# Optimization experiments

Hardware: AMD Instinct MI355X
Metric: run time of the kernel (lower is better)

## Reference

```python
import jax, jax.numpy as jnp
import numpy as np

N, F, D, E, L, T = 20000, 512, 256, 200000, 3, 2  # nodes, raw feat, hidden, edges/etype, layers, etypes


def _layernorm(x, g, b, eps=1e-5):
    mu = jnp.mean(x, axis=-1, keepdims=True)
    var = jnp.mean(jnp.square(x - mu), axis=-1, keepdims=True)
    return (x - mu) * jax.lax.rsqrt(var + eps) * g + b


def setup_inputs() -> dict:
    key = jax.random.key(0)
    ks = jax.random.split(key, 12)
    s = 0.02
    return {
        "x": jax.random.normal(ks[0], (N, F), dtype=jnp.float32),
        "src": jax.random.randint(ks[1], (T, E), 0, N, dtype=jnp.int32),
        "dst": jax.random.randint(ks[2], (T, E), 0, N, dtype=jnp.int32),
        # HeteroLinear (single ntype)
        "Wlin": jax.random.normal(ks[3], (D, F), dtype=jnp.float32) * s,
        "blin": jnp.zeros((D,), dtype=jnp.float32),
        # stacked per-layer, per-etype SAGEConv('pool') params
        "Wpool": jax.random.normal(ks[4], (L, T, D, D), dtype=jnp.float32) * s,
        "bpool": jnp.zeros((L, T, D), dtype=jnp.float32),
        "Wself": jax.random.normal(ks[5], (L, T, D, D), dtype=jnp.float32) * s,
        "Wneigh": jax.random.normal(ks[6], (L, T, D, D), dtype=jnp.float32) * s,
        "bconv": jnp.zeros((L, T, D), dtype=jnp.float32),
        "gamma": jnp.ones((L, T, D), dtype=jnp.float32),
        "beta": jnp.zeros((L, T, D), dtype=jnp.float32),
    }


def reference(x, src, dst, Wlin, blin, Wpool, bpool, Wself, Wneigh, bconv, gamma, beta):
    n = x.shape[0]
    # HeteroLinear: raw features -> embed
    h = x @ Wlin.T + blin
    for l in range(L):
        out = None
        for t in range(T):  # per edge-type SAGEConv, aggregator='pool'
            hp = jax.nn.relu(h @ Wpool[l, t].T + bpool[l, t])        # fc_pool + relu on src nodes
            m = hp[src[t]]                                            # gather [E, D]
            neigh = jax.ops.segment_max(m, dst[t], num_segments=n)    # max-pool reduce
            neigh = jnp.where(jnp.isneginf(neigh), 0.0, neigh)        # zero-in-degree -> 0 (DGL)
            rst = h @ Wself[l, t].T + neigh @ Wneigh[l, t].T + bconv[l, t]
            if l < L - 1:
                rst = jax.nn.relu(rst)                                # activation before norm
            rst = _layernorm(rst, gamma[l, t], beta[l, t])
            out = rst if out is None else out + rst                   # HeteroGraphConv 'sum'
        h = out
    return h
```

## Files before the change

kernel.cpp:

```cpp
#include <hip/hip_runtime.h>

#define N_NODES 20000
#define F_IN    512
#define D_H     256
#define E_EDGES 200000
#define L_LAYERS 3
#define T_ETYPES 2
#define NBANDS  157
#define M_PAD   (NBANDS * 128)

typedef __attribute__((ext_vector_type(8))) short bf16x8;
typedef __attribute__((ext_vector_type(4))) float f32x4;

__device__ __forceinline__ unsigned short f2b(float f) {
    unsigned int u = __float_as_uint(f);
    u = (u + 0x7FFFu + ((u >> 16) & 1u)) >> 16;
    return (unsigned short)u;
}
__device__ __forceinline__ unsigned int pack2(float a, float b) {
    return (unsigned int)f2b(a) | ((unsigned int)f2b(b) << 16);
}

__device__ __forceinline__ void gload16(const unsigned short* g, unsigned short* l)
{
    __builtin_amdgcn_global_load_lds(
        (const __attribute__((address_space(1))) void*)g,
        (__attribute__((address_space(3))) void*)l, 16, 0, 0);
}

__device__ __forceinline__ size_t slab_addr(int row, int col, int kslabs)
{
    return ((size_t)(row >> 7) * kslabs + (col >> 5)) * 4096
         + (((row >> 4) & 7) << 9) + (((col >> 3) & 3) << 7)
         + ((row & 15) << 3) + (col & 7);
}

__device__ __forceinline__ void shufg8(const float* __restrict__ s,
                                       unsigned short* __restrict__ d,
                                       int NO, int Mreal, int K, int o8)
{
    const int matsz8 = (NO * K) >> 3;
    const int mat = o8 / matsz8;
    const int rem = o8 - mat * matsz8;
    const int dst = rem << 3;
    const int slab = dst >> 12;
    const int w = dst & 4095;
    const int spr = K >> 5;
    const int slab_n = slab / spr, slab_k = slab - slab_n * spr;
    int row = slab_n * 128 + (((w >> 9) & 7) << 4) + ((w >> 3) & 15);
    if (row >= Mreal) row = Mreal - 1;
    const int kk = ((w >> 7) & 3) << 3;
    const size_t soff = (size_t)mat * Mreal * K + (size_t)row * K + slab_k * 32 + kk;
    const float4 a = *(const float4*)(s + soff);
    const float4 b = *(const float4*)(s + soff + 4);
    uint4 u;
    u.x = pack2(a.x, a.y); u.y = pack2(a.z, a.w);
    u.z = pack2(b.x, b.y); u.w = pack2(b.z, b.w);
    *(uint4*)(d + (size_t)mat * NO * K + dst) = u;
}

__global__ __launch_bounds__(256) void prep_kernel(
    const float* __restrict__ x,  unsigned short* __restrict__ xb, int nx8,
    const float* __restrict__ s0, unsigned short* __restrict__ d0, int NO0, int K0, int n08,
    const float* __restrict__ s1, unsigned short* __restrict__ d1, int NO1, int K1, int n18,
    const float* __restrict__ s2, unsigned short* __restrict__ d2, int NO2, int K2, int n28,
    const float* __restrict__ s3, unsigned short* __restrict__ d3, int NO3, int K3, int n38)
{
    int i = blockIdx.x * 256 + threadIdx.x;
    if (i < nx8) { shufg8(x, xb, M_PAD, N_NODES, F_IN, i); return; }
    i -= nx8;
    if (i < n08) { shufg8(s0, d0, NO0, NO0, K0, i); return; }
    if ((i -= n08) < n18) { shufg8(s1, d1, NO1, NO1, K1, i); return; }
    if ((i -= n18) < n28) { shufg8(s2, d2, NO2, NO2, K2, i); return; }
    if ((i -= n28) < n38) { shufg8(s3, d3, NO3, NO3, K3, i); return; }
}

template <int NSTEPS, int CS, int SLABOUT>
__global__ __launch_bounds__(512) void gemm_lds(
    const unsigned short* __restrict__ A,
    const unsigned short* __restrict__ Wf,
    const float* __restrict__ bias, unsigned short* __restrict__ Cout,
    int M, int ldc, int relu)
{
    __shared__ __align__(16) unsigned short As[3][4096];
    __shared__ __align__(16) unsigned short Bs[3][4096];
    const int tid = threadIdx.x, lane = tid & 63;
    const int w = tid >> 6, wm = w >> 2, wn = w & 3;
    const int id = blockIdx.x;
    const int g = id / (8 * CS), rem = id - g * (8 * CS);
    const int cs = rem >> 3, bmi = (g << 3) | (rem & 7);
    const int MB = (M + 127) >> 7;
    if (bmi >= MB) return;
    const int bm = bmi * 128;
    const unsigned short* slab0 = Wf + (((size_t)cs * NSTEPS) << 12);
    const unsigned short* abase = A + (((size_t)bmi * NSTEPS) << 12) + (size_t)tid * 8;
    const unsigned short* bsrc = slab0 + (size_t)tid * 8;

    const int cbase = cs * 128 + wn * 32 + (lane & 15);
    float bj[2];
#pragma unroll
    for (int j = 0; j < 2; ++j) bj[j] = bias[cbase + j * 16];
    asm volatile("" ::: "memory");

    f32x4 acc[4][2] = {};

#define GL_STAGE(S, BUF) do { \
    gload16(abase + (((size_t)(S)) << 12), &As[BUF][(size_t)tid * 8]); \
    gload16(bsrc + (((size_t)(S)) << 12), &Bs[BUF][(size_t)tid * 8]); \
} while (0)

    GL_STAGE(0, 0);
    GL_STAGE(1, 1);
#pragma unroll
    for (int s = 0; s < NSTEPS; ++s) {
        if (s + 1 < NSTEPS) asm volatile("s_waitcnt vmcnt(2)" ::: "memory");
        else                asm volatile("s_waitcnt vmcnt(0)" ::: "memory");
        __builtin_amdgcn_s_barrier();
        asm volatile("" ::: "memory");
        if (s + 2 < NSTEPS) GL_STAGE(s + 2, (s + 2) % 3);
        const int buf = s % 3;
        bf16x8 a[4], b[2];
#pragma unroll
        for (int mi = 0; mi < 4; ++mi)
            a[mi] = *(const bf16x8*)((const char*)As[buf] + ((wm * 4 + mi) << 10) + lane * 16);
#pragma unroll
        for (int j = 0; j < 2; ++j)
            b[j] = *(const bf16x8*)((const char*)Bs[buf] + ((wn * 2 + j) << 10) + lane * 16);
#pragma unroll
        for (int mi = 0; mi < 4; ++mi)
#pragma unroll
            for (int j = 0; j < 2; ++j)
                acc[mi][j] = __builtin_amdgcn_mfma_f32_16x16x32_bf16(a[mi], b[j], acc[mi][j], 0, 0, 0);
    }
#undef GL_STAGE

    const int rb = bm + wm * 64 + ((lane >> 4) << 2);
#pragma unroll
    for (int j = 0; j < 2; ++j) {
#pragma unroll
        for (int mi = 0; mi < 4; ++mi)
#pragma unroll
            for (int r = 0; r < 4; ++r) {
                const int row = rb + mi * 16 + r;
                if (row < M) {
                    float v = acc[mi][j][r] + bj[j];
                    if (relu) v = fmaxf(v, 0.f);
                    if (SLABOUT)
                        Cout[slab_addr(row, cbase + j * 16, 8)] = f2b(v);
                    else
                        Cout[(size_t)row * ldc + cbase + j * 16] = f2b(v);
                }
            }
    }
}

template <int RELU>
__global__ __launch_bounds__(512) void tail_gemm(
    const unsigned short* __restrict__ h,
    const unsigned short* __restrict__ neigh,
    const unsigned short* __restrict__ Ws,
    const unsigned short* __restrict__ Wn,
    const float* __restrict__ bias,
    float* __restrict__ R)
{
    __shared__ __align__(16) unsigned short As[3][4096];
    __shared__ __align__(16) unsigned short Bs[3][4096];
    const int tid = threadIdx.x, lane = tid & 63;
    const int w = tid >> 6, wm = w >> 2, wn = w & 3;
    const int id = blockIdx.x;
    const int g = id >> 5, rem = id & 31;
    const int cs = rem >> 3, bmi = (g << 3) | (rem & 7);
    if (bmi >= NBANDS) return;
    const int bm = bmi * 128;
    const int e  = cs >> 1;
    const unsigned short* Bself  = Ws + (size_t)e * 65536 + (cs & 1) * 32768;
    const unsigned short* Bneigh = Wn + (size_t)e * 65536 + (cs & 1) * 32768;
    const unsigned short* ah = h + (((size_t)bmi * 8) << 12) + (size_t)tid * 8;
    const unsigned short* an = neigh + (((size_t)bmi * 16 + e * 8) << 12) + (size_t)tid * 8;

    const int cbase = cs * 128 + wn * 32 + (lane & 15);
    float bj[2];
#pragma unroll
    for (int j = 0; j < 2; ++j) bj[j] = bias[cbase + j * 16];
    asm volatile("" ::: "memory");

    f32x4 acc[4][2] = {};

#define TG_STAGE(S, BUF) do { \
    const unsigned short* as_ = ((S) < 8) ? (ah + (((size_t)(S)) << 12)) \
                                          : (an + (((size_t)((S) - 8)) << 12)); \
    gload16(as_, &As[BUF][(size_t)tid * 8]); \
    const unsigned short* bs_ = (((S) < 8) ? (Bself + ((S) << 12)) \
                                           : (Bneigh + (((S) - 8) << 12))) \
                                + (size_t)tid * 8; \
    gload16(bs_, &Bs[BUF][(size_t)tid * 8]); \
} while (0)

    TG_STAGE(0, 0);
    TG_STAGE(1, 1);
#pragma unroll
    for (int s = 0; s < 16; ++s) {
        if (s + 1 < 16) asm volatile("s_waitcnt vmcnt(2)" ::: "memory");
        else            asm volatile("s_waitcnt vmcnt(0)" ::: "memory");
        __builtin_amdgcn_s_barrier();
        asm volatile("" ::: "memory");
        if (s + 2 < 16) TG_STAGE(s + 2, (s + 2) % 3);
        const int buf = s % 3;
        bf16x8 a[4], b[2];
#pragma unroll
        for (int mi = 0; mi < 4; ++mi)
            a[mi] = *(const bf16x8*)((const char*)As[buf] + ((wm * 4 + mi) << 10) + lane * 16);
#pragma unroll
        for (int j = 0; j < 2; ++j)
            b[j] = *(const bf16x8*)((const char*)Bs[buf] + ((wn * 2 + j) << 10) + lane * 16);
#pragma unroll
        for (int mi = 0; mi < 4; ++mi)
#pragma unroll
            for (int j = 0; j < 2; ++j)
                acc[mi][j] = __builtin_amdgcn_mfma_f32_16x16x32_bf16(a[mi], b[j], acc[mi][j], 0, 0, 0);
    }
#undef TG_STAGE

    const int rb = bm + wm * 64 + ((lane >> 4) << 2);
#pragma unroll
    for (int j = 0; j < 2; ++j) {
#pragma unroll
        for (int mi = 0; mi < 4; ++mi)
#pragma unroll
            for (int r = 0; r < 4; ++r) {
                const int row = rb + mi * 16 + r;
                if (row < N_NODES) {
                    float v = acc[mi][j][r] + bj[j];
                    if (RELU) v = fmaxf(v, 0.f);
                    R[(size_t)row * 512 + cbase + j * 16] = v;
                }
            }
    }
}

template <int LAST>
__global__ __launch_bounds__(256) void ln_sum_kernel(
    const float* __restrict__ R,
    const float* __restrict__ gamma,
    const float* __restrict__ beta,
    void* __restrict__ outp)
{
    const int row  = blockIdx.x * 4 + (threadIdx.x >> 6);
    const int lane = threadIdx.x & 63;
    const float4 v0 = ((const float4*)R)[(size_t)row * 128 + lane];
    const float4 v1 = ((const float4*)R)[(size_t)row * 128 + 64 + lane];
    float s0 = v0.x + v0.y + v0.z + v0.w;
    float q0 = v0.x * v0.x + v0.y * v0.y + v0.z * v0.z + v0.w * v0.w;
    float s1 = v1.x + v1.y + v1.z + v1.w;
    float q1 = v1.x * v1.x + v1.y * v1.y + v1.z * v1.z + v1.w * v1.w;
#pragma unroll
    for (int o = 1; o < 64; o <<= 1) {
        s0 += __shfl_xor(s0, o); q0 += __shfl_xor(q0, o);
        s1 += __shfl_xor(s1, o); q1 += __shfl_xor(q1, o);
    }
    const float m0 = s0 * (1.f / 256.f), m1 = s1 * (1.f / 256.f);
    const float i0 = rsqrtf(q0 * (1.f / 256.f) - m0 * m0 + 1e-5f);
    const float i1 = rsqrtf(q1 * (1.f / 256.f) - m1 * m1 + 1e-5f);
    const float4 g0 = ((const float4*)gamma)[lane];
    const float4 b0 = ((const float4*)beta)[lane];
    const float4 g1 = ((const float4*)(gamma + 256))[lane];
    const float4 b1 = ((const float4*)(beta + 256))[lane];
    const float o0 = (v0.x - m0) * i0 * g0.x + b0.x + (v1.x - m1) * i1 * g1.x + b1.x;
    const float o1 = (v0.y - m0) * i0 * g0.y + b0.y + (v1.y - m1) * i1 * g1.y + b1.y;
    const float o2 = (v0.z - m0) * i0 * g0.z + b0.z + (v1.z - m1) * i1 * g1.z + b1.z;
    const float o3 = (v0.w - m0) * i0 * g0.w + b0.w + (v1.w - m1) * i1 * g1.w + b1.w;
    if (LAST) {
        ((float4*)outp)[(size_t)row * 64 + lane] = make_float4(o0, o1, o2, o3);
    } else {
        ushort4 u;
        u.x = f2b(o0); u.y = f2b(o1); u.z = f2b(o2); u.w = f2b(o3);
        *(ushort4*)((unsigned short*)outp + slab_addr(row, lane * 4, 8)) = u;
    }
}

__global__ __launch_bounds__(256) void count_deg_kernel(
    const int* __restrict__ dst, int* __restrict__ cnt, int E2)
{
    int e = blockIdx.x * 256 + threadIdx.x;
    if (e < E2) {
        const int base = (e >= E_EDGES) ? N_NODES : 0;
        atomicAdd(&cnt[base + dst[e]], 1);
    }
}

__global__ __launch_bounds__(256) void scanA_kernel(
    const int* __restrict__ cnt, int* __restrict__ incl, int* __restrict__ bsum, int n)
{
    __shared__ int tmp[256];
    const int tid = threadIdx.x;
    const int i = blockIdx.x * 256 + tid;
    const int v = (i < n) ? cnt[i] : 0;
    tmp[tid] = v;
    __syncthreads();
#pragma unroll
    for (int o = 1; o < 256; o <<= 1) {
        const int t = (tid >= o) ? tmp[tid - o] : 0;
        __syncthreads();
        tmp[tid] += t;
        __syncthreads();
    }
    if (i < n) incl[i] = tmp[tid];
    if (tid == 255) bsum[blockIdx.x] = tmp[255];
}

__global__ __launch_bounds__(256) void scanB_kernel(int* __restrict__ bsum, int nb)
{
    __shared__ int tmp[256];
    const int tid = threadIdx.x;
    const int v = (tid < nb) ? bsum[tid] : 0;
    tmp[tid] = v;
    __syncthreads();
#pragma unroll
    for (int o = 1; o < 256; o <<= 1) {
        const int t = (tid >= o) ? tmp[tid - o] : 0;
        __syncthreads();
        tmp[tid] += t;
        __syncthreads();
    }
    if (tid < nb) bsum[tid] = tmp[tid] - v;
}

__global__ __launch_bounds__(256) void scanC_kernel(
    const int* __restrict__ cnt, const int* __restrict__ incl,
    const int* __restrict__ bsum, int* __restrict__ off, int* __restrict__ cursor, int n)
{
    const int i = blockIdx.x * 256 + threadIdx.x;
    if (i < n) {
        const int e = incl[i] + bsum[blockIdx.x];
        off[i + 1] = e;
        cursor[i] = e - cnt[i];
    }
    if (i == 0) off[0] = 0;
}

__global__ __launch_bounds__(256) void fill_csr_kernel(
    const int* __restrict__ src, const int* __restrict__ dst,
    int* __restrict__ cursor, int* __restrict__ esrc, int E2)
{
    int e = blockIdx.x * 256 + threadIdx.x;
    if (e < E2) {
        const int base = (e >= E_EDGES) ? N_NODES : 0;
        const int pos = atomicAdd(&cursor[base + dst[e]], 1);
        esrc[pos] = src[e];
    }
}

__device__ __forceinline__ ushort4 umax4(ushort4 a, ushort4 b)
{
    a.x = a.x > b.x ? a.x : b.x;
    a.y = a.y > b.y ? a.y : b.y;
    a.z = a.z > b.z ? a.z : b.z;
    a.w = a.w > b.w ? a.w : b.w;
    return a;
}

__global__ __launch_bounds__(256) void seg_max_kernel(
    const unsigned short* __restrict__ hp, const int* __restrict__ off,
    const int* __restrict__ esrc, unsigned short* __restrict__ neigh)
{
    const int g = blockIdx.x * 4 + (threadIdx.x >> 6);
    if (g >= 2 * N_NODES) return;
    const int t = (g >= N_NODES) ? 1 : 0;
    const int node = g - t * N_NODES;
    const int lane = threadIdx.x & 63;
    const int co = t * D_H + lane * 4;
    const int e0 = off[g], e1 = off[g + 1];
    ushort4 acc = make_ushort4(0, 0, 0, 0);
    int e = e0;
    for (; e + 4 <= e1; e += 4) {
        const int s0 = esrc[e + 0], s1 = esrc[e + 1];
        const int s2 = esrc[e + 2], s3 = esrc[e + 3];
        const ushort4 v0 = *(const ushort4*)(hp + (size_t)s0 * 512 + co);
        const ushort4 v1 = *(const ushort4*)(hp + (size_t)s1 * 512 + co);
        const ushort4 v2 = *(const ushort4*)(hp + (size_t)s2 * 512 + co);
        const ushort4 v3 = *(const ushort4*)(hp + (size_t)s3 * 512 + co);
        acc = umax4(umax4(umax4(acc, v0), umax4(v1, v2)), v3);
    }
    for (; e < e1; ++e)
        acc = umax4(acc, *(const ushort4*)(hp + (size_t)esrc[e] * 512 + co));
    *(ushort4*)(neigh + slab_addr(node, co, 16)) = acc;
}

extern "C" void kernel_launch(void* const* d_in, const int* in_sizes, int n_in,
                              void* d_out, int out_size, void* d_ws, size_t ws_size,
                              hipStream_t stream)
{
    const float* x      = (const float*)d_in[0];
    const int*   src    = (const int*)d_in[1];
    const int*   dst    = (const int*)d_in[2];
    const float* Wlin   = (const float*)d_in[3];
    const float* blin   = (const float*)d_in[4];
    const float* Wpool  = (const float*)d_in[5];
    const float* bpool  = (const float*)d_in[6];
    const float* Wself  = (const float*)d_in[7];
    const float* Wneigh = (const float*)d_in[8];
    const float* bconv  = (const float*)d_in[9];
    const float* gamma  = (const float*)d_in[10];
    const float* beta   = (const float*)d_in[11];

    char* p = (char*)d_ws;
    unsigned short* hp_b    = (unsigned short*)p; p += (size_t)N_NODES * 512 * 2;
    unsigned short* neigh_b = (unsigned short*)p; p += (size_t)M_PAD * 512 * 2;
    unsigned short* h_a     = (unsigned short*)p; p += (size_t)M_PAD * 256 * 2;
    unsigned short* h_b     = (unsigned short*)p; p += (size_t)M_PAD * 256 * 2;
    unsigned short* xb      = (unsigned short*)p; p += (size_t)M_PAD * F_IN * 2;
    float*          Rbuf    = (float*)p;          p += (size_t)N_NODES * 512 * 4;
    unsigned short* wlin_f  = (unsigned short*)p; p += (size_t)D_H * F_IN * 2;
    const size_t WSZ = (size_t)L_LAYERS * T_ETYPES * D_H * D_H;
    unsigned short* wpool_f = (unsigned short*)p; p += WSZ * 2;
    unsigned short* wself_f = (unsigned short*)p; p += WSZ * 2;
    unsigned short* wneigh_f= (unsigned short*)p; p += WSZ * 2;
    int* ip = (int*)p;
    const int NT = T_ETYPES * N_NODES;
    int* cnt    = ip; ip += NT;
    int* incl   = ip; ip += NT;
    int* off    = ip; ip += NT + 1;
    int* cursor = ip; ip += NT;
    int* esrc   = ip; ip += T_ETYPES * E_EDGES;
    int* bsum   = ip; ip += 256;

    const dim3 blk(256);
    const dim3 blk512(512);
    const int E2 = T_ETYPES * E_EDGES;
    const dim3 e2grid((E2 + 255) / 256);
    const int nScanBlk = (NT + 255) / 256;

    {
        const int nx8  = M_PAD * F_IN / 8;
        const int nl8  = D_H * F_IN / 8;
        const int nw8  = (int)(WSZ / 8);
        const int tot  = nx8 + nl8 + 3 * nw8;
        prep_kernel<<<dim3((tot + 255) / 256), blk, 0, stream>>>(
            x, xb, nx8,
            Wlin, wlin_f, D_H, F_IN, nl8,
            Wpool, wpool_f, T_ETYPES * D_H, D_H, nw8,
            Wself, wself_f, D_H, D_H, nw8,
            Wneigh, wneigh_f, D_H, D_H, nw8);
    }

    hipMemsetAsync(cnt, 0, (size_t)NT * sizeof(int), stream);
    count_deg_kernel<<<e2grid, blk, 0, stream>>>(dst, cnt, E2);
    scanA_kernel<<<dim3(nScanBlk), blk, 0, stream>>>(cnt, incl, bsum, NT);
    scanB_kernel<<<dim3(1), blk, 0, stream>>>(bsum, nScanBlk);
    scanC_kernel<<<dim3(nScanBlk), blk, 0, stream>>>(cnt, incl, bsum, off, cursor, NT);
    fill_csr_kernel<<<e2grid, blk, 0, stream>>>(src, dst, cursor, esrc, E2);

    const int MGRP = (NBANDS + 7) / 8;

    gemm_lds<16, 2, 1><<<dim3(MGRP * 16), blk512, 0, stream>>>(
        xb, wlin_f, blin, h_a, N_NODES, D_H, 0);

    unsigned short* h = h_a;
    unsigned short* hn = h_b;
    const dim3 sgrid((2 * N_NODES + 3) / 4);
    const dim3 lngrid(N_NODES / 4);
    for (int l = 0; l < L_LAYERS; ++l) {
        gemm_lds<8, 4, 0><<<dim3(MGRP * 32), blk512, 0, stream>>>(
            h, wpool_f + (size_t)l * T_ETYPES * D_H * D_H,
            bpool + (size_t)l * T_ETYPES * D_H, hp_b, N_NODES, T_ETYPES * D_H, 1);
        seg_max_kernel<<<sgrid, blk, 0, stream>>>(hp_b, off, esrc, neigh_b);
        const size_t wlo = (size_t)l * T_ETYPES * D_H * D_H;
        const size_t blo = (size_t)l * T_ETYPES * D_H;
        if (l < L_LAYERS - 1) {
            tail_gemm<1><<<dim3(MGRP * 32), blk512, 0, stream>>>(
                h, neigh_b, wself_f + wlo, wneigh_f + wlo, bconv + blo, Rbuf);
            ln_sum_kernel<0><<<lngrid, blk, 0, stream>>>(
                Rbuf, gamma + blo, beta + blo, hn);
        } else {
            tail_gemm<0><<<dim3(MGRP * 32), blk512, 0, stream>>>(
                h, neigh_b, wself_f + wlo, wneigh_f + wlo, bconv + blo, Rbuf);
            ln_sum_kernel<1><<<lngrid, blk, 0, stream>>>(
                Rbuf, gamma + blo, beta + blo, d_out);
        }
        unsigned short* tmp = h; h = hn; hn = tmp;
    }
}
```

Baseline: 387.9 us.

## Fuse layer pipeline into one cooperative persistent kernel with grid syncs

Replaces the per-layer sequence of GEMM, segment-max, tail GEMM and layernorm launches with a single cooperative mega-kernel. It runs 512 persistent blocks that loop over tiles and separate the stages with grid-wide syncs. The aim is to remove launch overhead and inter-kernel gaps across the roughly 13 stage launches. In exchange it adds grid-sync cost, tile-loop imbalance with a fixed 512-block grid, and lower occupancy. If the cooperative launch fails, it falls back to separate kernels built from the same device functions.

```diff
diff --git a/kernel.cpp b/kernel.cpp
--- a/kernel.cpp
+++ b/kernel.cpp
@@ -1,4 +1,7 @@
 #include <hip/hip_runtime.h>
+#include <hip/hip_cooperative_groups.h>
+
+namespace cg = cooperative_groups;
 
 #define N_NODES 20000
 #define F_IN    512
@@ -11,17 +14,18 @@
 
 typedef __attribute__((ext_vector_type(8))) short bf16x8;
 typedef __attribute__((ext_vector_type(4))) float f32x4;
-
-__device__ __forceinline__ unsigned short f2b(float f) {
+typedef unsigned short u16;
+
+__device__ __forceinline__ u16 f2b(float f) {
     unsigned int u = __float_as_uint(f);
     u = (u + 0x7FFFu + ((u >> 16) & 1u)) >> 16;
-    return (unsigned short)u;
+    return (u16)u;
 }
 __device__ __forceinline__ unsigned int pack2(float a, float b) {
     return (unsigned int)f2b(a) | ((unsigned int)f2b(b) << 16);
 }
 
-__device__ __forceinline__ void gload16(const unsigned short* g, unsigned short* l)
+__device__ __forceinline__ void gload16(const u16* g, u16* l)
 {
     __builtin_amdgcn_global_load_lds(
         (const __attribute__((address_space(1))) void*)g,
@@ -36,7 +40,7 @@
 }
 
 __device__ __forceinline__ void shufg8(const float* __restrict__ s,
-                                       unsigned short* __restrict__ d,
+                                       u16* __restrict__ d,
                                        int NO, int Mreal, int K, int o8)
 {
     const int matsz8 = (NO * K) >> 3;
@@ -60,11 +64,11 @@
 }
 
 __global__ __launch_bounds__(256) void prep_kernel(
-    const float* __restrict__ x,  unsigned short* __restrict__ xb, int nx8,
-    const float* __restrict__ s0, unsigned short* __restrict__ d0, int NO0, int K0, int n08,
-    const float* __restrict__ s1, unsigned short* __restrict__ d1, int NO1, int K1, int n18,
-    const float* __restrict__ s2, unsigned short* __restrict__ d2, int NO2, int K2, int n28,
-    const float* __restrict__ s3, unsigned short* __restrict__ d3, int NO3, int K3, int n38)
+    const float* __restrict__ x,  u16* __restrict__ xb, int nx8,
+    const float* __restrict__ s0, u16* __restrict__ d0, int NO0, int K0, int n08,
+    const float* __restrict__ s1, u16* __restrict__ d1, int NO1, int K1, int n18,
+    const float* __restrict__ s2, u16* __restrict__ d2, int NO2, int K2, int n28,
+    const float* __restrict__ s3, u16* __restrict__ d3, int NO3, int K3, int n38)
 {
     int i = blockIdx.x * 256 + threadIdx.x;
     if (i < nx8) { shufg8(x, xb, M_PAD, N_NODES, F_IN, i); return; }
@@ -75,207 +79,305 @@
     if ((i -= n28) < n38) { shufg8(s3, d3, NO3, NO3, K3, i); return; }
 }
 
+
 template <int NSTEPS, int CS, int SLABOUT>
-__global__ __launch_bounds__(512) void gemm_lds(
-    const unsigned short* __restrict__ A,
-    const unsigned short* __restrict__ Wf,
-    const float* __restrict__ bias, unsigned short* __restrict__ Cout,
-    int M, int ldc, int relu)
-{
-    __shared__ __align__(16) unsigned short As[3][4096];
-    __shared__ __align__(16) unsigned short Bs[3][4096];
+__device__ __forceinline__ void dev_gemm(
+    const u16* __restrict__ A, const u16* __restrict__ Wf,
+    const float* __restrict__ bias, u16* __restrict__ Cout,
+    int ldc, int relu, int nid, int grid, int bid,
+    u16 (*As)[4096], u16 (*Bs)[4096])
+{
     const int tid = threadIdx.x, lane = tid & 63;
     const int w = tid >> 6, wm = w >> 2, wn = w & 3;
-    const int id = blockIdx.x;
-    const int g = id / (8 * CS), rem = id - g * (8 * CS);
-    const int cs = rem >> 3, bmi = (g << 3) | (rem & 7);
-    const int MB = (M + 127) >> 7;
-    if (bmi >= MB) return;
-    const int bm = bmi * 128;
-    const unsigned short* slab0 = Wf + (((size_t)cs * NSTEPS) << 12);
-    const unsigned short* abase = A + (((size_t)bmi * NSTEPS) << 12) + (size_t)tid * 8;
-    const unsigned short* bsrc = slab0 + (size_t)tid * 8;
-
-    const int cbase = cs * 128 + wn * 32 + (lane & 15);
-    float bj[2];
-#pragma unroll
-    for (int j = 0; j < 2; ++j) bj[j] = bias[cbase + j * 16];
-    asm volatile("" ::: "memory");
-
-    f32x4 acc[4][2] = {};
-
-#define GL_STAGE(S, BUF) do { \
-    gload16(abase + (((size_t)(S)) << 12), &As[BUF][(size_t)tid * 8]); \
-    gload16(bsrc + (((size_t)(S)) << 12), &Bs[BUF][(size_t)tid * 8]); \
-} while (0)
-
-    GL_STAGE(0, 0);
-    GL_STAGE(1, 1);
-#pragma unroll
-    for (int s = 0; s < NSTEPS; ++s) {
-        if (s + 1 < NSTEPS) asm volatile("s_waitcnt vmcnt(2)" ::: "memory");
-        else                asm volatile("s_waitcnt vmcnt(0)" ::: "memory");
-        __builtin_amdgcn_s_barrier();
-        asm volatile("" ::: "memory");
-        if (s + 2 < NSTEPS) GL_STAGE(s + 2, (s + 2) % 3);
-        const int buf = s % 3;
-        bf16x8 a[4], b[2];
-#pragma unroll
-        for (int mi = 0; mi < 4; ++mi)
-            a[mi] = *(const bf16x8*)((const char*)As[buf] + ((wm * 4 + mi) << 10) + lane * 16);
-#pragma unroll
-        for (int j = 0; j < 2; ++j)
-            b[j] = *(const bf16x8*)((const char*)Bs[buf] + ((wn * 2 + j) << 10) + lane * 16);
-#pragma unroll
-        for (int mi = 0; mi < 4; ++mi)
-#pragma unroll
-            for (int j = 0; j < 2; ++j)
-                acc[mi][j] = __builtin_amdgcn_mfma_f32_16x16x32_bf16(a[mi], b[j], acc[mi][j], 0, 0, 0);
-    }
-#undef GL_STAGE
-
-    const int rb = bm + wm * 64 + ((lane >> 4) << 2);
-#pragma unroll
-    for (int j = 0; j < 2; ++j) {
-#pragma unroll
-        for (int mi = 0; mi < 4; ++mi)
-#pragma unroll
-            for (int r = 0; r < 4; ++r) {
-                const int row = rb + mi * 16 + r;
-                if (row < M) {
-                    float v = acc[mi][j][r] + bj[j];
-                    if (relu) v = fmaxf(v, 0.f);
-                    if (SLABOUT)
-                        Cout[slab_addr(row, cbase + j * 16, 8)] = f2b(v);
-                    else
-                        Cout[(size_t)row * ldc + cbase + j * 16] = f2b(v);
+    for (int id = bid; id < nid; id += grid) {
+        const int g = id / (8 * CS), rem = id - g * (8 * CS);
+        const int cs = rem >> 3, bmi = (g << 3) | (rem & 7);
+        if (bmi < NBANDS) {
+            const int bm = bmi * 128;
+            const u16* abase = A + (((size_t)bmi * NSTEPS) << 12) + (size_t)tid * 8;
+            const u16* bsrc = Wf + (((size_t)cs * NSTEPS) << 12) + (size_t)tid * 8;
+            const int cbase = cs * 128 + wn * 32 + (lane & 15);
+            float bj0 = bias[cbase], bj1 = bias[cbase + 16];
+            asm volatile("" ::: "memory");
+            f32x4 acc[4][2] = {};
+            gload16(abase, &As[0][(size_t)tid * 8]);
+            gload16(bsrc, &Bs[0][(size_t)tid * 8]);
+            gload16(abase + 4096, &As[1][(size_t)tid * 8]);
+            gload16(bsrc + 4096, &Bs[1][(size_t)tid * 8]);
+#pragma unroll
+            for (int s = 0; s < NSTEPS; ++s) {
+                if (s + 1 < NSTEPS) asm volatile("s_waitcnt vmcnt(2)" ::: "memory");
+                else                asm volatile("s_waitcnt vmcnt(0)" ::: "memory");
+                __builtin_amdgcn_s_barrier();
+                asm volatile("" ::: "memory");
+                if (s + 2 < NSTEPS) {
+                    gload16(abase + (((size_t)(s + 2)) << 12), &As[(s + 2) % 3][(size_t)tid * 8]);
+                    gload16(bsrc + (((size_t)(s + 2)) << 12), &Bs[(s + 2) % 3][(size_t)tid * 8]);
                 }
-            }
-    }
-}
-
-template <int RELU>
-__global__ __launch_bounds__(512) void tail_gemm(
-    const unsigned short* __restrict__ h,
-    const unsigned short* __restrict__ neigh,
-    const unsigned short* __restrict__ Ws,
-    const unsigned short* __restrict__ Wn,
-    const float* __restrict__ bias,
-    float* __restrict__ R)
-{
-    __shared__ __align__(16) unsigned short As[3][4096];
-    __shared__ __align__(16) unsigned short Bs[3][4096];
+                const int buf = s % 3;
+                bf16x8 av[4], bv[2];
+#pragma unroll
+                for (int mi = 0; mi < 4; ++mi)
+                    av[mi] = *(const bf16x8*)((const char*)As[buf] + ((wm * 4 + mi) << 10) + lane * 16);
+#pragma unroll
+                for (int j = 0; j < 2; ++j)
+                    bv[j] = *(const bf16x8*)((const char*)Bs[buf] + ((wn * 2 + j) << 10) + lane * 16);
+#pragma unroll
+                for (int mi = 0; mi < 4; ++mi)
+#pragma unroll
+                    for (int j = 0; j < 2; ++j)
+                        acc[mi][j] = __builtin_amdgcn_mfma_f32_16x16x32_bf16(av[mi], bv[j], acc[mi][j], 0, 0, 0);
+            }
+            const int rb = bm + wm * 64 + ((lane >> 4) << 2);
+#pragma unroll
+            for (int j = 0; j < 2; ++j) {
+                const float bj = j ? bj1 : bj0;
+#pragma unroll
+                for (int mi = 0; mi < 4; ++mi)
+#pragma unroll
+                    for (int r = 0; r < 4; ++r) {
+                        const int row = rb + mi * 16 + r;
+                        if (row < N_NODES) {
+                            float v = acc[mi][j][r] + bj;
+                            if (relu) v = fmaxf(v, 0.f);
+                            if (SLABOUT)
+                                Cout[slab_addr(row, cbase + j * 16, 8)] = f2b(v);
+                            else
+                                Cout[(size_t)row * ldc + cbase + j * 16] = f2b(v);
+                        }
+                    }
+            }
+        }
+        __syncthreads();
+    }
+}
+
+__device__ __forceinline__ void dev_tail(
+    const u16* __restrict__ h, const u16* __restrict__ neigh,
+    const u16* __restrict__ Ws, const u16* __restrict__ Wn,
+    const float* __restrict__ bias, int relu, float* __restrict__ R,
+    int nid, int grid, int bid, u16 (*As)[4096], u16 (*Bs)[4096])
+{
     const int tid = threadIdx.x, lane = tid & 63;
     const int w = tid >> 6, wm = w >> 2, wn = w & 3;
-    const int id = blockIdx.x;
-    const int g = id >> 5, rem = id & 31;
-    const int cs = rem >> 3, bmi = (g << 3) | (rem & 7);
-    if (bmi >= NBANDS) return;
-    const int bm = bmi * 128;
-    const int e  = cs >> 1;
-    const unsigned short* Bself  = Ws + (size_t)e * 65536 + (cs & 1) * 32768;
-    const unsigned short* Bneigh = Wn + (size_t)e * 65536 + (cs & 1) * 32768;
-    const unsigned short* ah = h + (((size_t)bmi * 8) << 12) + (size_t)tid * 8;
-    const unsigned short* an = neigh + (((size_t)bmi * 16 + e * 8) << 12) + (size_t)tid * 8;
-
-    const int cbase = cs * 128 + wn * 32 + (lane & 15);
-    float bj[2];
-#pragma unroll
-    for (int j = 0; j < 2; ++j) bj[j] = bias[cbase + j * 16];
-    asm volatile("" ::: "memory");
-
-    f32x4 acc[4][2] = {};
-
+    for (int id = bid; id < nid; id += grid) {
+        const int g = id >> 5, rem = id & 31;
+        const int cs = rem >> 3, bmi = (g << 3) | (rem & 7);
+        if (bmi < NBANDS) {
+            const int bm = bmi * 128;
+            const int e = cs >> 1;
+            const u16* Bself  = Ws + (size_t)e * 65536 + (cs & 1) * 32768 + (size_t)tid * 8;
+            const u16* Bneigh = Wn + (size_t)e * 65536 + (cs & 1) * 32768 + (size_t)tid * 8;
+            const u16* ah = h + (((size_t)bmi * 8) << 12) + (size_t)tid * 8;
+            const u16* an = neigh + (((size_t)bmi * 16 + e * 8) << 12) + (size_t)tid * 8;
+            const int cbase = cs * 128 + wn * 32 + (lane & 15);
+            float bj0 = bias[cbase], bj1 = bias[cbase + 16];
+            asm volatile("" ::: "memory");
+            f32x4 acc[4][2] = {};
 #define TG_STAGE(S, BUF) do { \
-    const unsigned short* as_ = ((S) < 8) ? (ah + (((size_t)(S)) << 12)) \
-                                          : (an + (((size_t)((S) - 8)) << 12)); \
+    const u16* as_ = ((S) < 8) ? (ah + (((size_t)(S)) << 12)) \
+                               : (an + (((size_t)((S) - 8)) << 12)); \
     gload16(as_, &As[BUF][(size_t)tid * 8]); \
-    const unsigned short* bs_ = (((S) < 8) ? (Bself + ((S) << 12)) \
-                                           : (Bneigh + (((S) - 8) << 12))) \
-                                + (size_t)tid * 8; \
+    const u16* bs_ = ((S) < 8) ? (Bself + (((size_t)(S)) << 12)) \
+                               : (Bneigh + (((size_t)((S) - 8)) << 12)); \
     gload16(bs_, &Bs[BUF][(size_t)tid * 8]); \
 } while (0)
-
-    TG_STAGE(0, 0);
-    TG_STAGE(1, 1);
-#pragma unroll
-    for (int s = 0; s < 16; ++s) {
-        if (s + 1 < 16) asm volatile("s_waitcnt vmcnt(2)" ::: "memory");
-        else            asm volatile("s_waitcnt vmcnt(0)" ::: "memory");
-        __builtin_amdgcn_s_barrier();
-        asm volatile("" ::: "memory");
-        if (s + 2 < 16) TG_STAGE(s + 2, (s + 2) % 3);
-        const int buf = s % 3;
-        bf16x8 a[4], b[2];
-#pragma unroll
-        for (int mi = 0; mi < 4; ++mi)
-            a[mi] = *(const bf16x8*)((const char*)As[buf] + ((wm * 4 + mi) << 10) + lane * 16);
-#pragma unroll
-        for (int j = 0; j < 2; ++j)
-            b[j] = *(const bf16x8*)((const char*)Bs[buf] + ((wn * 2 + j) << 10) + lane * 16);
-#pragma unroll
-        for (int mi = 0; mi < 4; ++mi)
-#pragma unroll
-            for (int j = 0; j < 2; ++j)
-                acc[mi][j] = __builtin_amdgcn_mfma_f32_16x16x32_bf16(a[mi], b[j], acc[mi][j], 0, 0, 0);
-    }
+            TG_STAGE(0, 0);
+            TG_STAGE(1, 1);
+#pragma unroll
+            for (int s = 0; s < 16; ++s) {
+                if (s + 1 < 16) asm volatile("s_waitcnt vmcnt(2)" ::: "memory");
+                else            asm volatile("s_waitcnt vmcnt(0)" ::: "memory");
+                __builtin_amdgcn_s_barrier();
+                asm volatile("" ::: "memory");
+                if (s + 2 < 16) TG_STAGE(s + 2, (s + 2) % 3);
+                const int buf = s % 3;
+                bf16x8 av[4], bv[2];
+#pragma unroll
+                for (int mi = 0; mi < 4; ++mi)
+                    av[mi] = *(const bf16x8*)((const char*)As[buf] + ((wm * 4 + mi) << 10) + lane * 16);
+#pragma unroll
+                for (int j = 0; j < 2; ++j)
+                    bv[j] = *(const bf16x8*)((const char*)Bs[buf] + ((wn * 2 + j) << 10) + lane * 16);
+#pragma unroll
+                for (int mi = 0; mi < 4; ++mi)
+#pragma unroll
+                    for (int j = 0; j < 2; ++j)
+                        acc[mi][j] = __builtin_amdgcn_mfma_f32_16x16x32_bf16(av[mi], bv[j], acc[mi][j], 0, 0, 0);
+            }
 #undef TG_STAGE
-
-    const int rb = bm + wm * 64 + ((lane >> 4) << 2);
-#pragma unroll
-    for (int j = 0; j < 2; ++j) {
-#pragma unroll
-        for (int mi = 0; mi < 4; ++mi)
-#pragma unroll
-            for (int r = 0; r < 4; ++r) {
-                const int row = rb + mi * 16 + r;
-                if (row < N_NODES) {
-                    float v = acc[mi][j][r] + bj[j];
-                    if (RELU) v = fmaxf(v, 0.f);
-                    R[(size_t)row * 512 + cbase + j * 16] = v;
-                }
-            }
+            const int rb = bm + wm * 64 + ((lane >> 4) << 2);
+#pragma unroll
+            for (int j = 0; j < 2; ++j) {
+                const float bj = j ? bj1 : bj0;
+#pragma unroll
+                for (int mi = 0; mi < 4; ++mi)
+#pragma unroll
+                    for (int r = 0; r < 4; ++r) {
+                        const int row = rb + mi * 16 + r;
+                        if (row < N_NODES) {
+                            float v = acc[mi][j][r] + bj;
+                            if (relu) v = fmaxf(v, 0.f);
+                            R[(size_t)row * 512 + cbase + j * 16] = v;
+                        }
+                    }
+            }
+        }
+        __syncthreads();
+    }
+}
+
+__device__ __forceinline__ ushort4 umax4(ushort4 a, ushort4 b)
+{
+    a.x = a.x > b.x ? a.x : b.x;
+    a.y = a.y > b.y ? a.y : b.y;
+    a.z = a.z > b.z ? a.z : b.z;
+    a.w = a.w > b.w ? a.w : b.w;
+    return a;
+}
+
+__device__ __forceinline__ void dev_segmax(
+    const u16* __restrict__ hp, const int* __restrict__ off,
+    const int* __restrict__ esrc, u16* __restrict__ neigh, int grid, int bid)
+{
+    const int tid = threadIdx.x;
+    const int lane = tid & 63;
+    for (int base = bid * 8; base < 2 * N_NODES; base += grid * 8) {
+        const int g = base + (tid >> 6);
+        if (g < 2 * N_NODES) {
+            const int t = (g >= N_NODES) ? 1 : 0;
+            const int node = g - t * N_NODES;
+            const int co = t * D_H + lane * 4;
+            const int e0 = off[g], e1 = off[g + 1];
+            ushort4 acc = make_ushort4(0, 0, 0, 0);
+            int e = e0;
+            for (; e + 4 <= e1; e += 4) {
+                const int s0 = esrc[e + 0], s1 = esrc[e + 1];
+                const int s2 = esrc[e + 2], s3 = esrc[e + 3];
+                const ushort4 v0 = *(const ushort4*)(hp + (size_t)s0 * 512 + co);
+                const ushort4 v1 = *(const ushort4*)(hp + (size_t)s1 * 512 + co);
+                const ushort4 v2 = *(const ushort4*)(hp + (size_t)s2 * 512 + co);
+                const ushort4 v3 = *(const ushort4*)(hp + (size_t)s3 * 512 + co);
+                acc = umax4(umax4(umax4(acc, v0), umax4(v1, v2)), v3);
+            }
+            for (; e < e1; ++e)
+                acc = umax4(acc, *(const ushort4*)(hp + (size_t)esrc[e] * 512 + co));
+            *(ushort4*)(neigh + slab_addr(node, co, 16)) = acc;
+        }
     }
 }
 
 template <int LAST>
-__global__ __launch_bounds__(256) void ln_sum_kernel(
-    const float* __restrict__ R,
-    const float* __restrict__ gamma,
-    const float* __restrict__ beta,
-    void* __restrict__ outp)
-{
-    const int row  = blockIdx.x * 4 + (threadIdx.x >> 6);
-    const int lane = threadIdx.x & 63;
-    const float4 v0 = ((const float4*)R)[(size_t)row * 128 + lane];
-    const float4 v1 = ((const float4*)R)[(size_t)row * 128 + 64 + lane];
-    float s0 = v0.x + v0.y + v0.z + v0.w;
-    float q0 = v0.x * v0.x + v0.y * v0.y + v0.z * v0.z + v0.w * v0.w;
-    float s1 = v1.x + v1.y + v1.z + v1.w;
-    float q1 = v1.x * v1.x + v1.y * v1.y + v1.z * v1.z + v1.w * v1.w;
-#pragma unroll
-    for (int o = 1; o < 64; o <<= 1) {
-        s0 += __shfl_xor(s0, o); q0 += __shfl_xor(q0, o);
-        s1 += __shfl_xor(s1, o); q1 += __shfl_xor(q1, o);
-    }
-    const float m0 = s0 * (1.f / 256.f), m1 = s1 * (1.f / 256.f);
-    const float i0 = rsqrtf(q0 * (1.f / 256.f) - m0 * m0 + 1e-5f);
-    const float i1 = rsqrtf(q1 * (1.f / 256.f) - m1 * m1 + 1e-5f);
-    const float4 g0 = ((const float4*)gamma)[lane];
-    const float4 b0 = ((const float4*)beta)[lane];
-    const float4 g1 = ((const float4*)(gamma + 256))[lane];
-    const float4 b1 = ((const float4*)(beta + 256))[lane];
-    const float o0 = (v0.x - m0) * i0 * g0.x + b0.x + (v1.x - m1) * i1 * g1.x + b1.x;
-    const float o1 = (v0.y - m0) * i0 * g0.y + b0.y + (v1.y - m1) * i1 * g1.y + b1.y;
-    const float o2 = (v0.z - m0) * i0 * g0.z + b0.z + (v1.z - m1) * i1 * g1.z + b1.z;
-    const float o3 = (v0.w - m0) * i0 * g0.w + b0.w + (v1.w - m1) * i1 * g1.w + b1.w;
-    if (LAST) {
-        ((float4*)outp)[(size_t)row * 64 + lane] = make_float4(o0, o1, o2, o3);
-    } else {
-        ushort4 u;
-        u.x = f2b(o0); u.y = f2b(o1); u.z = f2b(o2); u.w = f2b(o3);
-        *(ushort4*)((unsigned short*)outp + slab_addr(row, lane * 4, 8)) = u;
-    }
+__device__ __forceinline__ void dev_ln(
+    const float* __restrict__ R, const float* __restrict__ gamma,
+    const float* __restrict__ beta, void* __restrict__ outp, int grid, int bid)
+{
+    const int tid = threadIdx.x;
+    const int lane = tid & 63;
+    for (int base = bid * 8; base < N_NODES; base += grid * 8) {
+        const int row = base + (tid >> 6);
+        if (row < N_NODES) {
+            const float4 v0 = ((const float4*)R)[(size_t)row * 128 + lane];
+            const float4 v1 = ((const float4*)R)[(size_t)row * 128 + 64 + lane];
+            float s0 = v0.x + v0.y + v0.z + v0.w;
+            float q0 = v0.x * v0.x + v0.y * v0.y + v0.z * v0.z + v0.w * v0.w;
+            float s1 = v1.x + v1.y + v1.z + v1.w;
+            float q1 = v1.x * v1.x + v1.y * v1.y + v1.z * v1.z + v1.w * v1.w;
+#pragma unroll
+            for (int o = 1; o < 64; o <<= 1) {
+                s0 += __shfl_xor(s0, o); q0 += __shfl_xor(q0, o);
+                s1 += __shfl_xor(s1, o); q1 += __shfl_xor(q1, o);
+            }
+            const float m0 = s0 * (1.f / 256.f), m1 = s1 * (1.f / 256.f);
+            const float i0 = rsqrtf(q0 * (1.f / 256.f) - m0 * m0 + 1e-5f);
+            const float i1 = rsqrtf(q1 * (1.f / 256.f) - m1 * m1 + 1e-5f);
+            const float4 g0 = ((const float4*)gamma)[lane];
+            const float4 b0 = ((const float4*)beta)[lane];
+            const float4 g1 = ((const float4*)(gamma + 256))[lane];
+            const float4 b1 = ((const float4*)(beta + 256))[lane];
+            const float o0 = (v0.x - m0) * i0 * g0.x + b0.x + (v1.x - m1) * i1 * g1.x + b1.x;
+            const float o1 = (v0.y - m0) * i0 * g0.y + b0.y + (v1.y - m1) * i1 * g1.y + b1.y;
+            const float o2 = (v0.z - m0) * i0 * g0.z + b0.z + (v1.z - m1) * i1 * g1.z + b1.z;
+            const float o3 = (v0.w - m0) * i0 * g0.w + b0.w + (v1.w - m1) * i1 * g1.w + b1.w;
+            if (LAST) {
+                ((float4*)outp)[(size_t)row * 64 + lane] = make_float4(o0, o1, o2, o3);
+            } else {
+                ushort4 u;
+                u.x = f2b(o0); u.y = f2b(o1); u.z = f2b(o2); u.w = f2b(o3);
+                *(ushort4*)((u16*)outp + slab_addr(row, lane * 4, 8)) = u;
+            }
+        }
+    }
+}
+
+struct MArgs {
+    const u16 *xb, *wlin, *wpool, *wself, *wneigh;
+    const float *blin, *bpool, *bconv, *gamma, *beta;
+    const int *off, *esrc;
+    u16 *h_a, *h_b, *hp, *neigh;
+    float *R;
+    float *dout;
+};
+
+__global__ __launch_bounds__(512, 4) void mega_kernel(MArgs a)
+{
+    __shared__ __align__(16) u16 As[3][4096];
+    __shared__ __align__(16) u16 Bs[3][4096];
+    cg::grid_group gg = cg::this_grid();
+    const int grid = gridDim.x, bid = blockIdx.x;
+    const int MGRP16 = ((NBANDS + 7) / 8) * 16;
+    const int MGRP32 = MGRP16 * 2;
+
+    dev_gemm<16, 2, 1>(a.xb, a.wlin, a.blin, a.h_a, 0, 0, MGRP16, grid, bid, As, Bs);
+    const u16* h = a.h_a;
+    u16* hn = a.h_b;
+    for (int l = 0; l < L_LAYERS; ++l) {
+        const size_t wlo = (size_t)l * T_ETYPES * D_H * D_H;
+        const size_t blo = (size_t)l * T_ETYPES * D_H;
+        gg.sync();
+        dev_gemm<8, 4, 0>(h, a.wpool + wlo, a.bpool + blo, a.hp,
+                          T_ETYPES * D_H, 1, MGRP32, grid, bid, As, Bs);
+        gg.sync();
+        dev_segmax(a.hp, a.off, a.esrc, a.neigh, grid, bid);
+        gg.sync();
+        dev_tail(h, a.neigh, a.wself + wlo, a.wneigh + wlo, a.bconv + blo,
+                 (l < L_LAYERS - 1) ? 1 : 0, a.R, MGRP32, grid, bid, As, Bs);
+        gg.sync();
+        if (l < L_LAYERS - 1) dev_ln<0>(a.R, a.gamma + blo, a.beta + blo, hn, grid, bid);
+        else                  dev_ln<1>(a.R, a.gamma + blo, a.beta + blo, a.dout, grid, bid);
+        u16* t = (u16*)h; h = hn; hn = t;
+    }
+}
+
+template <int NSTEPS, int CS, int SLABOUT>
+__global__ __launch_bounds__(512) void k_gemm(
+    const u16* A, const u16* Wf, const float* bias, u16* C, int ldc, int relu, int nid)
+{
+    __shared__ __align__(16) u16 As[3][4096];
+    __shared__ __align__(16) u16 Bs[3][4096];
+    dev_gemm<NSTEPS, CS, SLABOUT>(A, Wf, bias, C, ldc, relu, nid, gridDim.x, blockIdx.x, As, Bs);
+}
+
+__global__ __launch_bounds__(512) void k_tail(
+    const u16* h, const u16* neigh, const u16* Ws, const u16* Wn,
+    const float* bias, int relu, float* R, int nid)
+{
+    __shared__ __align__(16) u16 As[3][4096];
+    __shared__ __align__(16) u16 Bs[3][4096];
+    dev_tail(h, neigh, Ws, Wn, bias, relu, R, nid, gridDim.x, blockIdx.x, As, Bs);
+}
+
+__global__ __launch_bounds__(512) void k_segmax(
+    const u16* hp, const int* off, const int* esrc, u16* neigh)
+{
+    dev_segmax(hp, off, esrc, neigh, gridDim.x, blockIdx.x);
+}
+
+template <int LAST>
+__global__ __launch_bounds__(512) void k_ln(
+    const float* R, const float* gamma, const float* beta, void* outp)
+{
+    dev_ln<LAST>(R, gamma, beta, outp, gridDim.x, blockIdx.x);
 }
 
 __global__ __launch_bounds__(256) void count_deg_kernel(
@@ -348,42 +450,6 @@
         const int pos = atomicAdd(&cursor[base + dst[e]], 1);
         esrc[pos] = src[e];
     }
-}
-
-__device__ __forceinline__ ushort4 umax4(ushort4 a, ushort4 b)
-{
-    a.x = a.x > b.x ? a.x : b.x;
-    a.y = a.y > b.y ? a.y : b.y;
-    a.z = a.z > b.z ? a.z : b.z;
-    a.w = a.w > b.w ? a.w : b.w;
-    return a;
-}
-
-__global__ __launch_bounds__(256) void seg_max_kernel(
-    const unsigned short* __restrict__ hp, const int* __restrict__ off,
-    const int* __restrict__ esrc, unsigned short* __restrict__ neigh)
-{
-    const int g = blockIdx.x * 4 + (threadIdx.x >> 6);
-    if (g >= 2 * N_NODES) return;
-    const int t = (g >= N_NODES) ? 1 : 0;
-    const int node = g - t * N_NODES;
-    const int lane = threadIdx.x & 63;
-    const int co = t * D_H + lane * 4;
-    const int e0 = off[g], e1 = off[g + 1];
-    ushort4 acc = make_ushort4(0, 0, 0, 0);
-    int e = e0;
-    for (; e + 4 <= e1; e += 4) {
-        const int s0 = esrc[e + 0], s1 = esrc[e + 1];
-        const int s2 = esrc[e + 2], s3 = esrc[e + 3];
-        const ushort4 v0 = *(const ushort4*)(hp + (size_t)s0 * 512 + co);
-        const ushort4 v1 = *(const ushort4*)(hp + (size_t)s1 * 512 + co);
-        const ushort4 v2 = *(const ushort4*)(hp + (size_t)s2 * 512 + co);
-        const ushort4 v3 = *(const ushort4*)(hp + (size_t)s3 * 512 + co);
-        acc = umax4(umax4(umax4(acc, v0), umax4(v1, v2)), v3);
-    }
-    for (; e < e1; ++e)
-        acc = umax4(acc, *(const ushort4*)(hp + (size_t)esrc[e] * 512 + co));
-    *(ushort4*)(neigh + slab_addr(node, co, 16)) = acc;
 }
 
 extern "C" void kernel_launch(void* const* d_in, const int* in_sizes, int n_in,
@@ -404,17 +470,17 @@
     const float* beta   = (const float*)d_in[11];
 
     char* p = (char*)d_ws;
-    unsigned short* hp_b    = (unsigned short*)p; p += (size_t)N_NODES * 512 * 2;
-    unsigned short* neigh_b = (unsigned short*)p; p += (size_t)M_PAD * 512 * 2;
-    unsigned short* h_a     = (unsigned short*)p; p += (size_t)M_PAD * 256 * 2;
-    unsigned short* h_b     = (unsigned short*)p; p += (size_t)M_PAD * 256 * 2;
-    unsigned short* xb      = (unsigned short*)p; p += (size_t)M_PAD * F_IN * 2;
-    float*          Rbuf    = (float*)p;          p += (size_t)N_NODES * 512 * 4;
-    unsigned short* wlin_f  = (unsigned short*)p; p += (size_t)D_H * F_IN * 2;
+    u16* hp_b    = (u16*)p; p += (size_t)N_NODES * 512 * 2;
+    u16* neigh_b = (u16*)p; p += (size_t)M_PAD * 512 * 2;
+    u16* h_a     = (u16*)p; p += (size_t)M_PAD * 256 * 2;
+    u16* h_b     = (u16*)p; p += (size_t)M_PAD * 256 * 2;
+    u16* xb      = (u16*)p; p += (size_t)M_PAD * F_IN * 2;
+    float* Rbuf  = (float*)p; p += (size_t)N_NODES * 512 * 4;
+    u16* wlin_f  = (u16*)p; p += (size_t)D_H * F_IN * 2;
     const size_t WSZ = (size_t)L_LAYERS * T_ETYPES * D_H * D_H;
-    unsigned short* wpool_f = (unsigned short*)p; p += WSZ * 2;
-    unsigned short* wself_f = (unsigned short*)p; p += WSZ * 2;
-    unsigned short* wneigh_f= (unsigned short*)p; p += WSZ * 2;
+    u16* wpool_f = (u16*)p; p += WSZ * 2;
+    u16* wself_f = (u16*)p; p += WSZ * 2;
+    u16* wneigh_f= (u16*)p; p += WSZ * 2;
     int* ip = (int*)p;
     const int NT = T_ETYPES * N_NODES;
     int* cnt    = ip; ip += NT;
@@ -425,7 +491,6 @@
     int* bsum   = ip; ip += 256;
 
     const dim3 blk(256);
-    const dim3 blk512(512);
     const int E2 = T_ETYPES * E_EDGES;
     const dim3 e2grid((E2 + 255) / 256);
     const int nScanBlk = (NT + 255) / 256;
@@ -450,33 +515,45 @@
     scanC_kernel<<<dim3(nScanBlk), blk, 0, stream>>>(cnt, incl, bsum, off, cursor, NT);
     fill_csr_kernel<<<e2grid, blk, 0, stream>>>(src, dst, cursor, esrc, E2);
 
-    const int MGRP = (NBANDS + 7) / 8;
-
-    gemm_lds<16, 2, 1><<<dim3(MGRP * 16), blk512, 0, stream>>>(
-        xb, wlin_f, blin, h_a, N_NODES, D_H, 0);
-
-    unsigned short* h = h_a;
-    unsigned short* hn = h_b;
-    const dim3 sgrid((2 * N_NODES + 3) / 4);
-    const dim3 lngrid(N_NODES / 4);
-    for (int l = 0; l < L_LAYERS; ++l) {
-        gemm_lds<8, 4, 0><<<dim3(MGRP * 32), blk512, 0, stream>>>(
-            h, wpool_f + (size_t)l * T_ETYPES * D_H * D_H,
-            bpool + (size_t)l * T_ETYPES * D_H, hp_b, N_NODES, T_ETYPES * D_H, 1);
-        seg_max_kernel<<<sgrid, blk, 0, stream>>>(hp_b, off, esrc, neigh_b);
-        const size_t wlo = (size_t)l * T_ETYPES * D_H * D_H;
-        const size_t blo = (size_t)l * T_ETYPES * D_H;
-        if (l < L_LAYERS - 1) {
-            tail_gemm<1><<<dim3(MGRP * 32), blk512, 0, stream>>>(
-                h, neigh_b, wself_f + wlo, wneigh_f + wlo, bconv + blo, Rbuf);
-            ln_sum_kernel<0><<<lngrid, blk, 0, stream>>>(
-                Rbuf, gamma + blo, beta + blo, hn);
-        } else {
-            tail_gemm<0><<<dim3(MGRP * 32), blk512, 0, stream>>>(
-                h, neigh_b, wself_f + wlo, wneigh_f + wlo, bconv + blo, Rbuf);
-            ln_sum_kernel<1><<<lngrid, blk, 0, stream>>>(
-                Rbuf, gamma + blo, beta + blo, d_out);
+    MArgs ma;
+    ma.xb = xb; ma.wlin = wlin_f; ma.wpool = wpool_f;
+    ma.wself = wself_f; ma.wneigh = wneigh_f;
+    ma.blin = blin; ma.bpool = bpool; ma.bconv = bconv;
+    ma.gamma = gamma; ma.beta = beta;
+    ma.off = off; ma.esrc = esrc;
+    ma.h_a = h_a; ma.h_b = h_b; ma.hp = hp_b; ma.neigh = neigh_b;
+    ma.R = Rbuf; ma.dout = (float*)d_out;
+
+    static bool coop_dead = false;
+    bool done = false;
+    if (!coop_dead) {
+        void* kp[] = { (void*)&ma };
+        hipError_t e = hipLaunchCooperativeKernel(
+            reinterpret_cast<const void*>(&mega_kernel),
+            dim3(512), dim3(512), kp, 0, stream);
+        if (e == hipSuccess) done = true;
+        else coop_dead = true;
+    }
+    if (!done) {
+        const int MGRP16 = ((NBANDS + 7) / 8) * 16, MGRP32 = MGRP16 * 2;
+        const dim3 blk512(512);
+        k_gemm<16, 2, 1><<<dim3(MGRP16), blk512, 0, stream>>>(
+            xb, wlin_f, blin, h_a, 0, 0, MGRP16);
+        u16* h = h_a; u16* hn = h_b;
+        for (int l = 0; l < L_LAYERS; ++l) {
+            const size_t wlo = (size_t)l * T_ETYPES * D_H * D_H;
+            const size_t blo = (size_t)l * T_ETYPES * D_H;
+            k_gemm<8, 4, 0><<<dim3(MGRP32), blk512, 0, stream>>>(
+                h, wpool_f + wlo, bpool + blo, hp_b, T_ETYPES * D_H, 1, MGRP32);
+            k_segmax<<<dim3(2 * N_NODES / 8), blk512, 0, stream>>>(hp_b, off, esrc, neigh_b);
+            k_tail<<<dim3(MGRP32), blk512, 0, stream>>>(
+                h, neigh_b, wself_f + wlo, wneigh_f + wlo, bconv + blo,
+                (l < L_LAYERS - 1) ? 1 : 0, Rbuf, MGRP32);
+            if (l < L_LAYERS - 1)
+                k_ln<0><<<dim3(N_NODES / 8), blk512, 0, stream>>>(Rbuf, gamma + blo, beta + blo, hn);
+            else
+                k_ln<1><<<dim3(N_NODES / 8), blk512, 0, stream>>>(Rbuf, gamma + blo, beta + blo, d_out);
+            u16* t = h; h = hn; hn = t;
         }
-        unsigned short* tmp = h; h = hn; hn = tmp;
-    }
-}
+    }
+}
```

Result: no change. 393.7 us (+1.5%).
